# Kernel optimization log

Hardware: AMD Instinct MI355X
Metric: run time of the kernel (lower is better)

The kernel has to match this reference:

```python
import jax, jax.numpy as jnp
import numpy as np

D_MODEL, D_STATE, D_CONV, D_INNER = 1024, 16, 4, 2048
BATCH, SEQLEN = 4, 2048


def setup_inputs() -> dict:
    key = jax.random.key(0)
    ks = jax.random.split(key, 8)
    x = jax.random.normal(ks[0], (BATCH, SEQLEN, D_MODEL), jnp.float32)
    W_in = jax.random.normal(ks[1], (D_MODEL, 2 * D_INNER), jnp.float32) / np.float32(np.sqrt(D_MODEL))
    conv_w = jax.random.normal(ks[2], (D_INNER, 1, D_CONV), jnp.float32) * np.float32(0.3)
    W_x = jax.random.normal(ks[3], (D_INNER, 2 * D_STATE), jnp.float32) / np.float32(np.sqrt(D_INNER))
    W_dt = jax.random.normal(ks[4], (D_STATE, D_INNER), jnp.float32) / np.float32(np.sqrt(D_STATE))
    b_dt = jax.random.normal(ks[5], (D_INNER,), jnp.float32) * np.float32(0.1)
    W_Bp = jax.random.normal(ks[6], (D_STATE, D_INNER), jnp.float32) / np.float32(np.sqrt(D_STATE))
    D_param = jnp.ones((D_INNER,), jnp.float32)
    W_out = jax.random.normal(ks[7], (D_INNER, D_MODEL), jnp.float32) / np.float32(np.sqrt(D_INNER))
    return {"x": x, "W_in": W_in, "conv_w": conv_w, "W_x": W_x,
            "W_dt": W_dt, "b_dt": b_dt, "W_Bp": W_Bp, "D_param": D_param,
            "W_out": W_out}


def _mamba_fwd(x, W_in, conv_w, W_x, W_dt, b_dt, W_Bp, D_param, W_out):
    B, L, _ = x.shape
    xz = x @ W_in                                   # [B,L,2*d_inner]
    xc, z = jnp.split(xz, 2, axis=-1)
    # causal depthwise conv1d (torch pads d_conv-1 both sides then slices [:L])
    xt = jnp.transpose(xc, (0, 2, 1))               # [B,d_inner,L]
    xt = jax.lax.conv_general_dilated(
        xt, conv_w,
        window_strides=(1,), padding=[(D_CONV - 1, 0)],
        dimension_numbers=("NCH", "OIH", "NCH"),
        feature_group_count=D_INNER)
    u = jax.nn.silu(jnp.transpose(xt, (0, 2, 1)))   # [B,L,d_inner]
    xp = u @ W_x                                    # [B,L,2*d_state]
    dt_raw, B_raw = jnp.split(xp, 2, axis=-1)
    dt = jax.nn.softplus(dt_raw @ W_dt + b_dt)      # [B,L,d_inner]
    Bp = B_raw @ W_Bp                               # [B,L,d_inner]
    dt = jnp.clip(dt, 1e-4, 1.0)
    # selective scan: h_t = h_{t-1}*(1-dt_t) + u_t*Bp_t (note: A is unused in source)
    ub = u * Bp
    def step(h, inp):
        d_t, ub_t = inp
        h = h * (1.0 - d_t) + ub_t
        return h, h
    _, ys = jax.lax.scan(step, jnp.zeros((B, D_INNER), x.dtype),
                         (jnp.transpose(dt, (1, 0, 2)), jnp.transpose(ub, (1, 0, 2))))
    y = jnp.transpose(ys, (1, 0, 2)) + D_param * u  # [B,L,d_inner]
    y = y * jax.nn.silu(z)
    return y @ W_out                                # [B,L,d_model]


def reference(x, W_in, conv_w, W_x, W_dt, b_dt, W_Bp, D_param, W_out):
    # dropout is identity in eval mode
    return _mamba_fwd(x, W_in, conv_w, W_x, W_dt, b_dt, W_Bp, D_param, W_out)
```

## Files before the change

kernel.cpp:

```cpp
#include <hip/hip_runtime.h>
#include <cstdint>
#include <cstddef>

#define DM   1024
#define DI   2048
#define SEQ  2048
#define NB   4
#define NTOK (NB*SEQ)
#define CCH  32
#define LC   (SEQ/CCH)
#define KS   8

typedef __attribute__((ext_vector_type(8))) short short8v;
typedef __attribute__((ext_vector_type(4))) float f32x4;
typedef unsigned short u16;
typedef unsigned int   u32;

__device__ __forceinline__ float silu_f(float x){ return x / (1.f + __expf(-x)); }

__device__ __forceinline__ float softplus_f(float x){
  return (x > 20.f) ? x : __logf(1.f + __expf(x));
}

__device__ __forceinline__ u16 f2bf(float f){
  union { float f; u32 u; } c; c.f = f;
  u32 u = c.u + 0x7FFFu + ((c.u >> 16) & 1u);
  return (u16)(u >> 16);
}
__device__ __forceinline__ float b2f(u16 b){
  union { u32 u; float f; } c; c.u = ((u32)b) << 16; return c.f;
}
__device__ __forceinline__ float lo2f(u32 v){ union { u32 u; float f; } c; c.u = v << 16; return c.f; }
__device__ __forceinline__ float hi2f(u32 v){ union { u32 u; float f; } c; c.u = v & 0xFFFF0000u; return c.f; }
__device__ __forceinline__ u32 pack2(float a, float b){ return (u32)f2bf(a) | ((u32)f2bf(b) << 16); }

__device__ __forceinline__ void gl16(const void* g, void* l){
  __builtin_amdgcn_global_load_lds((const __attribute__((address_space(1))) void*)g,
                                   (__attribute__((address_space(3))) void*)l, 16, 0, 0);
}

__global__ __launch_bounds__(256) void cvtk(const float4* __restrict__ in,
                                            u16* __restrict__ outp, int n4)
{
  int i = blockIdx.x * 256 + threadIdx.x;
  if (i < n4) {
    float4 v = in[i];
    *(uint2*)(outp + (size_t)i * 4) = make_uint2(pack2(v.x, v.y), pack2(v.z, v.w));
  }
}

__global__ __launch_bounds__(256) void transcvt(
    const float* __restrict__ W, u16* __restrict__ Wt, int R, int Cn)
{
  __shared__ float t[64][65];
  const int tid = threadIdx.x;
  const int bx = blockIdx.x, by = blockIdx.y;
  const int lr4 = tid >> 6;
  const int lc  = tid & 63;
  #pragma unroll
  for (int p = 0; p < 16; ++p) {
    int lr = p * 4 + lr4;
    t[lr][lc] = W[(size_t)(by * 64 + lr) * Cn + bx * 64 + lc];
  }
  __syncthreads();
  #pragma unroll
  for (int p = 0; p < 16; ++p) {
    int orr = p * 4 + lr4;
    Wt[(size_t)(bx * 64 + orr) * R + by * 64 + lc] = f2bf(t[lc][orr]);
  }
}

__global__ __launch_bounds__(256) void prep_smallw(
    const float* __restrict__ W_x, const float* __restrict__ W_dt,
    const float* __restrict__ W_Bp, u16* __restrict__ Wxt, u16* __restrict__ Wbig)
{
  int i = blockIdx.x * 256 + threadIdx.x;
  if (i < 32 * DI) {
    int j = i >> 11, c = i & (DI - 1);
    Wxt[i] = f2bf(W_x[c * 32 + j]);
  }
  int i2 = i - 32 * DI;
  if (i2 >= 0 && i2 < 2 * DI * 32) {
    int n = i2 >> 5, k = i2 & 31;
    float v;
    if (n < DI) v = (k < 16) ? W_dt[k * DI + n] : 0.f;
    else        v = (k >= 16) ? W_Bp[(k - 16) * DI + (n - DI)] : 0.f;
    Wbig[i2] = f2bf(v);
  }
}

template<int NT, int OBF16>
__global__ __launch_bounds__(256, 2) void gemm2b(
    const u16* __restrict__ A, const u16* __restrict__ Bt,
    void* C0v, void* C1v, int K, int split, int ldc)
{
  __shared__ __align__(16) u16 Ab[2][128 * 64];
  __shared__ __align__(16) u16 Bb[2][128 * 64];
  const int tid = threadIdx.x, lane = tid & 63, w = tid >> 6;
  const int wm = w >> 1, wn = w & 1;
  const int bm = blockIdx.y * 128, bn = blockIdx.x * 128;

  const int srow8 = tid >> 3;
  const int kc = ((tid & 7) ^ (srow8 & 7)) << 3;
  const u16* Ag = A  + (size_t)(bm + srow8) * K + kc;
  const u16* Bg = Bt + (size_t)(bn + srow8) * K + kc;

  const int lq = lane >> 4, l15 = lane & 15;
  const int co0 = ((lq    ) ^ (l15 & 7)) << 3;
  const int co1 = ((lq + 4) ^ (l15 & 7)) << 3;
  const int abase = (wm * 64 + l15) * 64;
  const int bbase = (wn * 64 + l15) * 64;

  f32x4 acc[4][4] = {};

  auto issue = [&](int t, int buf) {
    const size_t k0 = (size_t)t << 6;
    #pragma unroll
    for (int q = 0; q < 4; ++q)
      gl16(Ag + (size_t)(q * 32) * K + k0, &Ab[buf][q * 2048 + tid * 8]);
    #pragma unroll
    for (int q = 0; q < 4; ++q)
      gl16(Bg + (size_t)(q * 32) * K + k0, &Bb[buf][q * 2048 + tid * 8]);
  };
  auto compute = [&](int buf) {
    const u16* Ac = Ab[buf];
    const u16* Bc = Bb[buf];
    short8v af[4], bf[4];
    #pragma unroll
    for (int ks = 0; ks < 2; ++ks) {
      const int co = ks ? co1 : co0;
      #pragma unroll
      for (int i = 0; i < 4; ++i) af[i] = *(const short8v*)&Ac[abase + i * 1024 + co];
      #pragma unroll
      for (int j = 0; j < 4; ++j) bf[j] = *(const short8v*)&Bc[bbase + j * 1024 + co];
      __builtin_amdgcn_s_setprio(1);
      #pragma unroll
      for (int i = 0; i < 4; ++i)
        #pragma unroll
        for (int j = 0; j < 4; ++j)
          acc[i][j] = __builtin_amdgcn_mfma_f32_16x16x32_bf16(af[i], bf[j], acc[i][j], 0, 0, 0);
      __builtin_amdgcn_s_setprio(0);
    }
  };

  issue(0, 0); issue(1, 1);
  #pragma unroll 1
  for (int t = 0; t < NT; ++t) {
    if (t + 1 < NT) asm volatile("s_waitcnt vmcnt(8)" ::: "memory");
    else            asm volatile("s_waitcnt vmcnt(0)" ::: "memory");
    __builtin_amdgcn_s_barrier(); __builtin_amdgcn_sched_barrier(0);
    compute(t & 1);
    __builtin_amdgcn_s_barrier(); __builtin_amdgcn_sched_barrier(0);
    if (t + 2 < NT) issue(t + 2, t & 1);
  }

  const bool left = (bn < split);
  const int cb = bn - (left ? 0 : split) + wn * 64 + l15;
  const int rb = bm + wm * 64 + lq * 4;
  if (OBF16) {
    u16* Cp = (u16*)(left ? C0v : C1v);
    #pragma unroll
    for (int i = 0; i < 4; ++i)
      #pragma unroll
      for (int j = 0; j < 4; ++j)
        #pragma unroll
        for (int r = 0; r < 4; ++r)
          Cp[(size_t)(rb + i * 16 + r) * ldc + cb + j * 16] = f2bf(acc[i][j][r]);
  } else {
    float* Cp = (float*)(left ? C0v : C1v);
    #pragma unroll
    for (int i = 0; i < 4; ++i)
      #pragma unroll
      for (int j = 0; j < 4; ++j)
        #pragma unroll
        for (int r = 0; r < 4; ++r)
          Cp[(size_t)(rb + i * 16 + r) * ldc + cb + j * 16] = acc[i][j][r];
  }
}

__global__ __launch_bounds__(256) void xp_gemm(
    const u16* __restrict__ A, const u16* __restrict__ Bt, float* __restrict__ xpp)
{
  __shared__ __align__(16) u16 Asm[128 * 32];
  __shared__ __align__(16) u16 Bsm[32 * 32];
  const int tid = threadIdx.x, lane = tid & 63, w = tid >> 6;
  const int bm = blockIdx.x * 128;
  const int kbase = blockIdx.y * (DI / KS);
  f32x4 acc[2][2] = {};
  const int srow = w * 32 + (lane >> 2);
  const int soct = lane & 3;
  const u16* Ap = A + (size_t)(bm + srow) * DI + kbase + soct * 8;
  const u16* Bp = Bt + (size_t)(lane >> 2) * DI + kbase + soct * 8;
  u16* As0 = &Asm[w * 1024];

  for (int k0 = 0; k0 < DI / KS; k0 += 32) {
    gl16(Ap + k0,                      As0);
    gl16(Ap + k0 + (size_t)16 * DI,    As0 + 512);
    if (w == 0) {
      gl16(Bp + k0,                    Bsm);
      gl16(Bp + k0 + (size_t)16 * DI,  Bsm + 512);
    }
    __syncthreads();
    short8v af[2], bf[2];
    #pragma unroll
    for (int i = 0; i < 2; ++i)
      af[i] = *(const short8v*)&Asm[(w * 32 + i * 16 + (lane & 15)) * 32 + (lane >> 4) * 8];
    #pragma unroll
    for (int j = 0; j < 2; ++j)
      bf[j] = *(const short8v*)&Bsm[(j * 16 + (lane & 15)) * 32 + (lane >> 4) * 8];
    #pragma unroll
    for (int i = 0; i < 2; ++i)
      #pragma unroll
      for (int j = 0; j < 2; ++j)
        acc[i][j] = __builtin_amdgcn_mfma_f32_16x16x32_bf16(af[i], bf[j], acc[i][j], 0, 0, 0);
    __syncthreads();
  }
  float* op = xpp + (size_t)blockIdx.y * NTOK * 32;
  const int rb = bm + w * 32 + (lane >> 4) * 4;
  const int cb = lane & 15;
  #pragma unroll
  for (int i = 0; i < 2; ++i)
    #pragma unroll
    for (int j = 0; j < 2; ++j)
      #pragma unroll
      for (int r = 0; r < 4; ++r)
        op[(size_t)(rb + i * 16 + r) * 32 + cb + j * 16] = acc[i][j][r];
}

__global__ __launch_bounds__(256) void xp_reduce(
    const float* __restrict__ xpp, u16* __restrict__ xpb)
{
  int i = blockIdx.x * 256 + threadIdx.x;
  float s = 0.f;
  #pragma unroll
  for (int k = 0; k < KS; ++k) s += xpp[(size_t)k * NTOK * 32 + i];
  xpb[i] = f2bf(s);
}

__global__ __launch_bounds__(256) void dtub_gemm(
    const u16* __restrict__ A, const u16* __restrict__ Bt,
    const float* __restrict__ b_dt, const u16* __restrict__ u,
    u16* __restrict__ dt_out, u16* __restrict__ ub_out)
{
  __shared__ __align__(16) u16 Asm[128 * 32];
  __shared__ __align__(16) u16 Bsm[128 * 32];
  const int tid = threadIdx.x, lane = tid & 63, w = tid >> 6;
  const int wm = w >> 1, wn = w & 1;
  const int bm = blockIdx.y * 128, bn = blockIdx.x * 128;
  const int srow = w * 32 + (lane >> 2);
  const int soct = lane & 3;
  u16* As0 = &Asm[w * 1024];
  u16* Bs0 = &Bsm[w * 1024];
  gl16(A  + (size_t)(bm + srow) * 32 + soct * 8,       As0);
  gl16(A  + (size_t)(bm + srow) * 32 + soct * 8 + 512, As0 + 512);
  gl16(Bt + (size_t)(bn + srow) * 32 + soct * 8,       Bs0);
  gl16(Bt + (size_t)(bn + srow) * 32 + soct * 8 + 512, Bs0 + 512);
  __syncthreads();
  f32x4 acc[4][4] = {};
  short8v afr[4], bfr[4];
  #pragma unroll
  for (int i = 0; i < 4; ++i) {
    afr[i] = *(const short8v*)&Asm[(wm * 64 + i * 16 + (lane & 15)) * 32 + (lane >> 4) * 8];
    bfr[i] = *(const short8v*)&Bsm[(wn * 64 + i * 16 + (lane & 15)) * 32 + (lane >> 4) * 8];
  }
  #pragma unroll
  for (int i = 0; i < 4; ++i)
    #pragma unroll
    for (int j = 0; j < 4; ++j)
      acc[i][j] = __builtin_amdgcn_mfma_f32_16x16x32_bf16(afr[i], bfr[j], acc[i][j], 0, 0, 0);

  const int rb = bm + wm * 64 + (lane >> 4) * 4;
  const int cb = bn + wn * 64 + (lane & 15);
  if (bn < DI) {
    float bd[4];
    #pragma unroll
    for (int j = 0; j < 4; ++j) bd[j] = b_dt[cb + j * 16];
    #pragma unroll
    for (int i = 0; i < 4; ++i)
      #pragma unroll
      for (int j = 0; j < 4; ++j)
        #pragma unroll
        for (int r = 0; r < 4; ++r) {
          float sp = softplus_f(acc[i][j][r] + bd[j]);
          sp = fminf(fmaxf(sp, 1e-4f), 1.0f);
          dt_out[(size_t)(rb + i * 16 + r) * DI + cb + j * 16] = f2bf(sp);
        }
  } else {
    const int cn = cb - DI;
    #pragma unroll
    for (int i = 0; i < 4; ++i)
      #pragma unroll
      for (int j = 0; j < 4; ++j)
        #pragma unroll
        for (int r = 0; r < 4; ++r) {
          size_t off = (size_t)(rb + i * 16 + r) * DI + cn + j * 16;
          ub_out[off] = f2bf(b2f(u[off]) * acc[i][j][r]);
        }
  }
}

__global__ __launch_bounds__(256) void conv_silu_k(
    const u16* __restrict__ xc, const float* __restrict__ cw, u16* __restrict__ u)
{
  int idx = blockIdx.x * 256 + threadIdx.x;
  int c = (idx & (DI / 2 - 1)) << 1;
  int r = idx >> 10;
  int t = r & (SEQ - 1);
  float4 w0 = ((const float4*)cw)[c];
  float4 w1 = ((const float4*)cw)[c + 1];
  const u16* base = xc + (size_t)r * DI + c;
  u32 v = *(const u32*)base;
  float a0 = w0.w * lo2f(v), a1 = w1.w * hi2f(v);
  if (t >= 1) { v = *(const u32*)(base - DI);     a0 += w0.z * lo2f(v); a1 += w1.z * hi2f(v); }
  if (t >= 2) { v = *(const u32*)(base - 2 * DI); a0 += w0.y * lo2f(v); a1 += w1.y * hi2f(v); }
  if (t >= 3) { v = *(const u32*)(base - 3 * DI); a0 += w0.x * lo2f(v); a1 += w1.x * hi2f(v); }
  *(u32*)(u + (size_t)r * DI + c) = pack2(silu_f(a0), silu_f(a1));
}

__global__ __launch_bounds__(256) void scan_p1(
    const u16* __restrict__ dt_, const u16* __restrict__ ub,
    float* __restrict__ P, float* __restrict__ S)
{
  int idx = blockIdx.x * 256 + threadIdx.x;
  int di = (idx & (DI / 2 - 1)) << 1;
  int bc = idx >> 10;
  int c  = bc & (CCH - 1);
  int b  = bc >> 5;
  size_t base = ((size_t)b * SEQ + (size_t)c * LC) * DI + di;
  float p0 = 1.f, s0 = 0.f, p1 = 1.f, s1 = 0.f;
  #pragma unroll 4
  for (int t = 0; t < LC; ++t) {
    size_t off = base + (size_t)t * DI;
    u32 dv = *(const u32*)(dt_ + off);
    u32 uv = *(const u32*)(ub + off);
    float a0 = 1.f - lo2f(dv), a1 = 1.f - hi2f(dv);
    s0 = s0 * a0 + lo2f(uv); p0 *= a0;
    s1 = s1 * a1 + hi2f(uv); p1 *= a1;
  }
  ((float2*)P)[idx] = make_float2(p0, p1);
  ((float2*)S)[idx] = make_float2(s0, s1);
}

__global__ __launch_bounds__(256) void scan_p2(
    const float* __restrict__ P, const float* __restrict__ S, float* __restrict__ Hin)
{
  int idx = blockIdx.x * 256 + threadIdx.x;
  int di = idx & (DI - 1);
  int b  = idx >> 11;
  float h = 0.f;
  #pragma unroll
  for (int c = 0; c < CCH; ++c) {
    size_t off = ((size_t)b * CCH + c) * DI + di;
    Hin[off] = h;
    h = h * P[off] + S[off];
  }
}

__global__ __launch_bounds__(256) void scan_p3(
    const u16* dt_, const u16* __restrict__ ub, const u16* __restrict__ u,
    const u16* __restrict__ z, const float* __restrict__ Dp_,
    const float* __restrict__ Hin, u16* y)
{
  int idx = blockIdx.x * 256 + threadIdx.x;
  int di = (idx & (DI / 2 - 1)) << 1;
  int bc = idx >> 10;
  int c  = bc & (CCH - 1);
  int b  = bc >> 5;
  float2 dp = ((const float2*)Dp_)[di >> 1];
  float2 h2 = ((const float2*)Hin)[idx];
  float h0 = h2.x, h1 = h2.y;
  size_t base = ((size_t)b * SEQ + (size_t)c * LC) * DI + di;
  #pragma unroll 4
  for (int t = 0; t < LC; ++t) {
    size_t off = base + (size_t)t * DI;
    u32 dv = *(const u32*)(dt_ + off);
    u32 uv = *(const u32*)(ub + off);
    u32 uu = *(const u32*)(u + off);
    u32 zv = *(const u32*)(z + off);
    h0 = h0 * (1.f - lo2f(dv)) + lo2f(uv);
    h1 = h1 * (1.f - hi2f(dv)) + hi2f(uv);
    float y0 = (h0 + dp.x * lo2f(uu)) * silu_f(lo2f(zv));
    float y1 = (h1 + dp.y * hi2f(uu)) * silu_f(hi2f(zv));
    *(u32*)(y + off) = pack2(y0, y1);
  }
}

extern "C" void kernel_launch(void* const* d_in, const int* in_sizes, int n_in,
                              void* d_out, int out_size, void* d_ws, size_t ws_size,
                              hipStream_t stream)
{
  const float* x     = (const float*)d_in[0];
  const float* W_in  = (const float*)d_in[1];
  const float* cw    = (const float*)d_in[2];
  const float* W_x   = (const float*)d_in[3];
  const float* W_dt  = (const float*)d_in[4];
  const float* b_dt  = (const float*)d_in[5];
  const float* W_Bp  = (const float*)d_in[6];
  const float* Dp    = (const float*)d_in[7];
  const float* W_out = (const float*)d_in[8];
  float* out = (float*)d_out;

  const size_t SZ = (size_t)NTOK * DI;
  float* w    = (float*)d_ws;
  float* bufA = w;
  float* bufB = w + SZ;
  float* bufC = w + 2 * SZ;
  float* bufD = w + 3 * SZ;

  u16* xcb  = (u16*)bufA;
  u16* zb   = (u16*)bufB;
  u16* wtob = zb + (size_t)NTOK * DI;
  u16* wxt  = wtob + (size_t)DM * DI;
  u16* wbig = wxt + (size_t)32 * DI;
  u16* xbf  = (u16*)bufC;
  u16* wtib = xbf + (size_t)NTOK * DM;
  u16* ubf  = (u16*)bufC;
  u16* ubb  = (u16*)bufD;

  const size_t PS = (size_t)NB * CCH * DI;
  float* Pbuf   = out;
  float* Sbuf   = out + PS;
  float* Hin    = out + 2 * PS;
  float* xppart = out + 3 * PS;
  u16*   xpb    = (u16*)(out + 3 * PS + (size_t)KS * NTOK * 32);
  (void)ws_size; (void)in_sizes; (void)n_in; (void)out_size;

  cvtk<<<(NTOK * DM / 4) / 256, 256, 0, stream>>>((const float4*)x, xbf, NTOK * DM / 4);
  transcvt<<<dim3((2 * DI) / 64, DM / 64), 256, 0, stream>>>(W_in, wtib, DM, 2 * DI);
  transcvt<<<dim3(DM / 64, DI / 64), 256, 0, stream>>>(W_out, wtob, DI, DM);
  prep_smallw<<<(32 * DI + 2 * DI * 32) / 256, 256, 0, stream>>>(W_x, W_dt, W_Bp, wxt, wbig);

  gemm2b<DM / 64, 1><<<dim3((2 * DI) / 128, NTOK / 128), 256, 0, stream>>>(
      xbf, wtib, (void*)xcb, (void*)zb, DM, DI, DI);

  conv_silu_k<<<(NTOK * DI / 2) / 256, 256, 0, stream>>>(xcb, cw, ubf);

  xp_gemm<<<dim3(NTOK / 128, KS), 256, 0, stream>>>(ubf, wxt, xppart);
  xp_reduce<<<(NTOK * 32) / 256, 256, 0, stream>>>(xppart, xpb);
  dtub_gemm<<<dim3((2 * DI) / 128, NTOK / 128), 256, 0, stream>>>(
      xpb, wbig, b_dt, ubf, xcb, ubb);

  scan_p1<<<(NB * CCH * DI / 2) / 256, 256, 0, stream>>>(xcb, ubb, Pbuf, Sbuf);
  scan_p2<<<(NB * DI) / 256, 256, 0, stream>>>(Pbuf, Sbuf, Hin);
  scan_p3<<<(NB * CCH * DI / 2) / 256, 256, 0, stream>>>(xcb, ubb, ubf, zb, Dp, Hin, xcb);

  gemm2b<DI / 64, 0><<<dim3(DM / 128, NTOK / 128), 256, 0, stream>>>(
      xcb, wtob, (void*)out, (void*)out, DI, DM, DM);
}
```

Measured before the change: 299.9 us.

## Remap GEMM blocks per XCD and widen elementwise/scan kernels to 4 channels

The two large GEMMs now use a 1D grid whose block IDs are remapped so each XCD (id & 7) works on a contiguous band of 8 row tiles. This aims to improve L2 reuse of A and B tiles on the chiplet design. Separately, the conv+silu and scan phase 1/3 kernels each process 4 channels per thread with 8-byte loads and stores instead of 2 channels with 4-byte accesses. That halves thread count, which cuts instruction overhead per byte but also lowers parallelism in the scan passes.

After: 307.6 us. +2.6%, slower.

```diff
diff --git a/kernel.cpp b/kernel.cpp
--- a/kernel.cpp
+++ b/kernel.cpp
@@ -89,7 +89,7 @@
   }
 }
 
-template<int NT, int OBF16>
+template<int NT, int LOG_NBX, int OBF16>
 __global__ __launch_bounds__(256, 2) void gemm2b(
     const u16* __restrict__ A, const u16* __restrict__ Bt,
     void* C0v, void* C1v, int K, int split, int ldc)
@@ -98,7 +98,10 @@
   __shared__ __align__(16) u16 Bb[2][128 * 64];
   const int tid = threadIdx.x, lane = tid & 63, w = tid >> 6;
   const int wm = w >> 1, wn = w & 1;
-  const int bm = blockIdx.y * 128, bn = blockIdx.x * 128;
+  const int id = blockIdx.x;
+  const int xcd = id & 7, slot = id >> 3;
+  const int bm = (xcd * 8 + (slot >> LOG_NBX)) * 128;
+  const int bn = (slot & ((1 << LOG_NBX) - 1)) * 128;
 
   const int srow8 = tid >> 3;
   const int kc = ((tid & 7) ^ (srow8 & 7)) << 3;
@@ -303,18 +306,25 @@
     const u16* __restrict__ xc, const float* __restrict__ cw, u16* __restrict__ u)
 {
   int idx = blockIdx.x * 256 + threadIdx.x;
-  int c = (idx & (DI / 2 - 1)) << 1;
-  int r = idx >> 10;
+  int c = (idx & (DI / 4 - 1)) << 2;
+  int r = idx >> 9;
   int t = r & (SEQ - 1);
-  float4 w0 = ((const float4*)cw)[c];
+  float4 w0 = ((const float4*)cw)[c + 0];
   float4 w1 = ((const float4*)cw)[c + 1];
+  float4 w2 = ((const float4*)cw)[c + 2];
+  float4 w3 = ((const float4*)cw)[c + 3];
   const u16* base = xc + (size_t)r * DI + c;
-  u32 v = *(const u32*)base;
-  float a0 = w0.w * lo2f(v), a1 = w1.w * hi2f(v);
-  if (t >= 1) { v = *(const u32*)(base - DI);     a0 += w0.z * lo2f(v); a1 += w1.z * hi2f(v); }
-  if (t >= 2) { v = *(const u32*)(base - 2 * DI); a0 += w0.y * lo2f(v); a1 += w1.y * hi2f(v); }
-  if (t >= 3) { v = *(const u32*)(base - 3 * DI); a0 += w0.x * lo2f(v); a1 += w1.x * hi2f(v); }
-  *(u32*)(u + (size_t)r * DI + c) = pack2(silu_f(a0), silu_f(a1));
+  uint2 v = *(const uint2*)base;
+  float a0 = w0.w * lo2f(v.x), a1 = w1.w * hi2f(v.x);
+  float a2 = w2.w * lo2f(v.y), a3 = w3.w * hi2f(v.y);
+  if (t >= 1) { v = *(const uint2*)(base - DI);
+    a0 += w0.z * lo2f(v.x); a1 += w1.z * hi2f(v.x); a2 += w2.z * lo2f(v.y); a3 += w3.z * hi2f(v.y); }
+  if (t >= 2) { v = *(const uint2*)(base - 2 * DI);
+    a0 += w0.y * lo2f(v.x); a1 += w1.y * hi2f(v.x); a2 += w2.y * lo2f(v.y); a3 += w3.y * hi2f(v.y); }
+  if (t >= 3) { v = *(const uint2*)(base - 3 * DI);
+    a0 += w0.x * lo2f(v.x); a1 += w1.x * hi2f(v.x); a2 += w2.x * lo2f(v.y); a3 += w3.x * hi2f(v.y); }
+  *(uint2*)(u + (size_t)r * DI + c) =
+      make_uint2(pack2(silu_f(a0), silu_f(a1)), pack2(silu_f(a2), silu_f(a3)));
 }
 
 __global__ __launch_bounds__(256) void scan_p1(
@@ -322,23 +332,27 @@
     float* __restrict__ P, float* __restrict__ S)
 {
   int idx = blockIdx.x * 256 + threadIdx.x;
-  int di = (idx & (DI / 2 - 1)) << 1;
-  int bc = idx >> 10;
+  int di = (idx & (DI / 4 - 1)) << 2;
+  int bc = idx >> 9;
   int c  = bc & (CCH - 1);
   int b  = bc >> 5;
   size_t base = ((size_t)b * SEQ + (size_t)c * LC) * DI + di;
   float p0 = 1.f, s0 = 0.f, p1 = 1.f, s1 = 0.f;
+  float p2 = 1.f, s2 = 0.f, p3 = 1.f, s3 = 0.f;
   #pragma unroll 4
   for (int t = 0; t < LC; ++t) {
     size_t off = base + (size_t)t * DI;
-    u32 dv = *(const u32*)(dt_ + off);
-    u32 uv = *(const u32*)(ub + off);
-    float a0 = 1.f - lo2f(dv), a1 = 1.f - hi2f(dv);
-    s0 = s0 * a0 + lo2f(uv); p0 *= a0;
-    s1 = s1 * a1 + hi2f(uv); p1 *= a1;
-  }
-  ((float2*)P)[idx] = make_float2(p0, p1);
-  ((float2*)S)[idx] = make_float2(s0, s1);
+    uint2 dv = *(const uint2*)(dt_ + off);
+    uint2 uv = *(const uint2*)(ub + off);
+    float a0 = 1.f - lo2f(dv.x), a1 = 1.f - hi2f(dv.x);
+    float a2 = 1.f - lo2f(dv.y), a3 = 1.f - hi2f(dv.y);
+    s0 = s0 * a0 + lo2f(uv.x); p0 *= a0;
+    s1 = s1 * a1 + hi2f(uv.x); p1 *= a1;
+    s2 = s2 * a2 + lo2f(uv.y); p2 *= a2;
+    s3 = s3 * a3 + hi2f(uv.y); p3 *= a3;
+  }
+  ((float4*)P)[idx] = make_float4(p0, p1, p2, p3);
+  ((float4*)S)[idx] = make_float4(s0, s1, s2, s3);
 }
 
 __global__ __launch_bounds__(256) void scan_p2(
@@ -362,26 +376,30 @@
     const float* __restrict__ Hin, u16* y)
 {
   int idx = blockIdx.x * 256 + threadIdx.x;
-  int di = (idx & (DI / 2 - 1)) << 1;
-  int bc = idx >> 10;
+  int di = (idx & (DI / 4 - 1)) << 2;
+  int bc = idx >> 9;
   int c  = bc & (CCH - 1);
   int b  = bc >> 5;
-  float2 dp = ((const float2*)Dp_)[di >> 1];
-  float2 h2 = ((const float2*)Hin)[idx];
-  float h0 = h2.x, h1 = h2.y;
+  float4 dp = ((const float4*)Dp_)[di >> 2];
+  float4 h4 = ((const float4*)Hin)[idx];
+  float h0 = h4.x, h1 = h4.y, h2 = h4.z, h3 = h4.w;
   size_t base = ((size_t)b * SEQ + (size_t)c * LC) * DI + di;
   #pragma unroll 4
   for (int t = 0; t < LC; ++t) {
     size_t off = base + (size_t)t * DI;
-    u32 dv = *(const u32*)(dt_ + off);
-    u32 uv = *(const u32*)(ub + off);
-    u32 uu = *(const u32*)(u + off);
-    u32 zv = *(const u32*)(z + off);
-    h0 = h0 * (1.f - lo2f(dv)) + lo2f(uv);
-    h1 = h1 * (1.f - hi2f(dv)) + hi2f(uv);
-    float y0 = (h0 + dp.x * lo2f(uu)) * silu_f(lo2f(zv));
-    float y1 = (h1 + dp.y * hi2f(uu)) * silu_f(hi2f(zv));
-    *(u32*)(y + off) = pack2(y0, y1);
+    uint2 dv = *(const uint2*)(dt_ + off);
+    uint2 uv = *(const uint2*)(ub + off);
+    uint2 uu = *(const uint2*)(u + off);
+    uint2 zv = *(const uint2*)(z + off);
+    h0 = h0 * (1.f - lo2f(dv.x)) + lo2f(uv.x);
+    h1 = h1 * (1.f - hi2f(dv.x)) + hi2f(uv.x);
+    h2 = h2 * (1.f - lo2f(dv.y)) + lo2f(uv.y);
+    h3 = h3 * (1.f - hi2f(dv.y)) + hi2f(uv.y);
+    float y0 = (h0 + dp.x * lo2f(uu.x)) * silu_f(lo2f(zv.x));
+    float y1 = (h1 + dp.y * hi2f(uu.x)) * silu_f(hi2f(zv.x));
+    float y2 = (h2 + dp.z * lo2f(uu.y)) * silu_f(lo2f(zv.y));
+    float y3 = (h3 + dp.w * hi2f(uu.y)) * silu_f(hi2f(zv.y));
+    *(uint2*)(y + off) = make_uint2(pack2(y0, y1), pack2(y2, y3));
   }
 }
 
@@ -430,20 +448,20 @@
   transcvt<<<dim3(DM / 64, DI / 64), 256, 0, stream>>>(W_out, wtob, DI, DM);
   prep_smallw<<<(32 * DI + 2 * DI * 32) / 256, 256, 0, stream>>>(W_x, W_dt, W_Bp, wxt, wbig);
 
-  gemm2b<DM / 64, 1><<<dim3((2 * DI) / 128, NTOK / 128), 256, 0, stream>>>(
+  gemm2b<DM / 64, 5, 1><<<2048, 256, 0, stream>>>(
       xbf, wtib, (void*)xcb, (void*)zb, DM, DI, DI);
 
-  conv_silu_k<<<(NTOK * DI / 2) / 256, 256, 0, stream>>>(xcb, cw, ubf);
+  conv_silu_k<<<(NTOK * DI / 4) / 256, 256, 0, stream>>>(xcb, cw, ubf);
 
   xp_gemm<<<dim3(NTOK / 128, KS), 256, 0, stream>>>(ubf, wxt, xppart);
   xp_reduce<<<(NTOK * 32) / 256, 256, 0, stream>>>(xppart, xpb);
   dtub_gemm<<<dim3((2 * DI) / 128, NTOK / 128), 256, 0, stream>>>(
       xpb, wbig, b_dt, ubf, xcb, ubb);
 
-  scan_p1<<<(NB * CCH * DI / 2) / 256, 256, 0, stream>>>(xcb, ubb, Pbuf, Sbuf);
+  scan_p1<<<(NB * CCH * DI / 4) / 256, 256, 0, stream>>>(xcb, ubb, Pbuf, Sbuf);
   scan_p2<<<(NB * DI) / 256, 256, 0, stream>>>(Pbuf, Sbuf, Hin);
-  scan_p3<<<(NB * CCH * DI / 2) / 256, 256, 0, stream>>>(xcb, ubb, ubf, zb, Dp, Hin, xcb);
-
-  gemm2b<DI / 64, 0><<<dim3(DM / 128, NTOK / 128), 256, 0, stream>>>(
+  scan_p3<<<(NB * CCH * DI / 4) / 256, 256, 0, stream>>>(xcb, ubb, ubf, zb, Dp, Hin, xcb);
+
+  gemm2b<DI / 64, 3, 0><<<512, 256, 0, stream>>>(
       xcb, wtob, (void*)out, (void*)out, DI, DM, DM);
 }
```
